# Performance work log

Measured on AMD Instinct MI355X. Metric: run time of the kernel, lower is better.

The kernel has to match this reference:

```python
import jax, jax.numpy as jnp
import numpy as np

EPS = 1e-5  # BatchNorm eps
B, T, D, H, C = 64, 1024, 128, 1024, 128


def _glorot(k, shape):
    lim = float(np.sqrt(6.0 / (shape[0] + shape[1])))
    return jax.random.uniform(k, shape, minval=-lim, maxval=lim, dtype=jnp.float32)


def _bn(x, g, b, m, v):
    # eval-mode BatchNorm1d over the channel (last) dim
    return (x - m) * (g * jax.lax.rsqrt(v + EPS)) + b


def _cell(x, h, c, Wih, Whh, bias):
    # PyTorch LSTM gate order: i, f, g, o
    z = x @ Wih.T + h @ Whh.T + bias
    i, f, g, o = jnp.split(z, 4, axis=-1)
    c = jax.nn.sigmoid(f) * c + jax.nn.sigmoid(i) * jnp.tanh(g)
    h = jax.nn.sigmoid(o) * jnp.tanh(c)
    return h, c


def setup_inputs() -> dict:
    key = jax.random.key(0)
    ks = jax.random.split(key, 24)
    d = {}
    d['x'] = jax.random.normal(ks[0], (B, T, D), dtype=jnp.float32)
    # input BN (eval mode running stats + affine)
    d['ibn_g'] = jnp.ones((D,), jnp.float32); d['ibn_b'] = jnp.zeros((D,), jnp.float32)
    d['ibn_m'] = 0.1 * jax.random.normal(ks[1], (D,), jnp.float32)
    d['ibn_v'] = jnp.ones((D,), jnp.float32)
    # encoder LSTM (2 layers)
    d['enc_Wih0'] = _glorot(ks[2], (4 * H, D)); d['enc_Whh0'] = _glorot(ks[3], (4 * H, H))
    d['enc_b0'] = jnp.zeros((4 * H,), jnp.float32)
    d['enc_Wih1'] = _glorot(ks[4], (4 * H, H)); d['enc_Whh1'] = _glorot(ks[5], (4 * H, H))
    d['enc_b1'] = jnp.zeros((4 * H,), jnp.float32)
    # decoder LSTM (2 layers), layer0 input = num_classes
    d['dec_Wih0'] = _glorot(ks[6], (4 * H, C)); d['dec_Whh0'] = _glorot(ks[7], (4 * H, H))
    d['dec_b0'] = jnp.zeros((4 * H,), jnp.float32)
    d['dec_Wih1'] = _glorot(ks[8], (4 * H, H)); d['dec_Whh1'] = _glorot(ks[9], (4 * H, H))
    d['dec_b1'] = jnp.zeros((4 * H,), jnp.float32)
    # hidden BN
    d['hbn_g'] = jnp.ones((H,), jnp.float32); d['hbn_b'] = jnp.zeros((H,), jnp.float32)
    d['hbn_m'] = 0.1 * jax.random.normal(ks[10], (H,), jnp.float32)
    d['hbn_v'] = jnp.ones((H,), jnp.float32)
    # fc head: Linear(H,H) -> BN -> ReLU -> (Dropout=identity in eval) -> Linear(H,C)
    d['fc1_W'] = _glorot(ks[11], (H, H)); d['fc1_b'] = jnp.zeros((H,), jnp.float32)
    d['fbn_g'] = jnp.ones((H,), jnp.float32); d['fbn_b'] = jnp.zeros((H,), jnp.float32)
    d['fbn_m'] = 0.1 * jax.random.normal(ks[12], (H,), jnp.float32)
    d['fbn_v'] = jnp.ones((H,), jnp.float32)
    d['fc2_W'] = _glorot(ks[13], (C, H)); d['fc2_b'] = jnp.zeros((C,), jnp.float32)
    return d


def reference(x, ibn_g, ibn_b, ibn_m, ibn_v,
              enc_Wih0, enc_Whh0, enc_b0, enc_Wih1, enc_Whh1, enc_b1,
              dec_Wih0, dec_Whh0, dec_b0, dec_Wih1, dec_Whh1, dec_b1,
              hbn_g, hbn_b, hbn_m, hbn_v,
              fc1_W, fc1_b, fbn_g, fbn_b, fbn_m, fbn_v, fc2_W, fc2_b):
    b, t, _ = x.shape
    h = enc_Whh0.shape[1]
    c_dim = fc2_W.shape[0]
    xn = _bn(x, ibn_g, ibn_b, ibn_m, ibn_v)  # (B,T,D), per-channel BN

    def enc_step(carry, xt):
        h0, c0, h1, c1 = carry
        h0, c0 = _cell(xt, h0, c0, enc_Wih0, enc_Whh0, enc_b0)
        h1, c1 = _cell(h0, h1, c1, enc_Wih1, enc_Whh1, enc_b1)
        return (h0, c0, h1, c1), None

    z = jnp.zeros((b, h), x.dtype)
    (h0, c0, h1, c1), _ = jax.lax.scan(enc_step, (z, z, z, z), jnp.swapaxes(xn, 0, 1))

    def dec_step(carry, _):
        d0, e0, d1, e1, y = carry
        d0, e0 = _cell(y, d0, e0, dec_Wih0, dec_Whh0, dec_b0)
        d1, e1 = _cell(d0, d1, e1, dec_Wih1, dec_Whh1, dec_b1)
        hb = _bn(d1, hbn_g, hbn_b, hbn_m, hbn_v)
        f1 = jax.nn.relu(_bn(hb @ fc1_W.T + fc1_b, fbn_g, fbn_b, fbn_m, fbn_v))
        pred = f1 @ fc2_W.T + fc2_b  # (B, C)
        return (d0, e0, d1, e1, pred), pred

    y0 = jnp.zeros((b, c_dim), x.dtype)
    _, preds = jax.lax.scan(dec_step, (h0, c0, h1, c1, y0), None, length=t)
    return jnp.swapaxes(preds, 0, 1)  # (B, T, C)
```

## Files before the change

### kernel.cpp

```cpp
#include <hip/hip_runtime.h>
#include <hip/hip_bf16.h>


typedef __hip_bfloat16 hbf16;
typedef __bf16 bf16x8 __attribute__((ext_vector_type(8)));
typedef float f32x4 __attribute__((ext_vector_type(4)));
#define DEVI static __device__ __forceinline__

#define PITCH 2056
#define PITCH0 1160
#define SLE 66048L
#define SLDATA 65536L

DEVI float sigf(float x) { return 1.0f / (1.0f + __expf(-x)); }

DEVI bf16x8 as_bf(f32x4 v) { union { f32x4 f; bf16x8 b; } u; u.f = v; return u.b; }

DEVI void st_u32_coh(void* p, unsigned int v) {
  __hip_atomic_store((unsigned int*)p, v, __ATOMIC_RELAXED, __HIP_MEMORY_SCOPE_AGENT);
}
DEVI void st_u64_coh(void* p, unsigned long long v) {
  __hip_atomic_store((unsigned long long*)p, v, __ATOMIC_RELAXED, __HIP_MEMORY_SCOPE_AGENT);
}
DEVI void st_f32_coh(float* p, float v) {
  __hip_atomic_store(p, v, __ATOMIC_RELAXED, __HIP_MEMORY_SCOPE_AGENT);
}
DEVI unsigned short bf_bits(float v) {
  union { __hip_bfloat16 b; unsigned short s; } u;
  u.b = __float2bfloat16(v);
  return u.s;
}

DEVI void ld32_wait(f32x4* b, const hbf16* ap) {
  asm volatile(
    "global_load_dwordx4 %0, %32, off sc0 sc1\n\t"
    "global_load_dwordx4 %1, %32, off offset:64 sc0 sc1\n\t"
    "global_load_dwordx4 %2, %32, off offset:128 sc0 sc1\n\t"
    "global_load_dwordx4 %3, %32, off offset:192 sc0 sc1\n\t"
    "global_load_dwordx4 %4, %32, off offset:256 sc0 sc1\n\t"
    "global_load_dwordx4 %5, %32, off offset:320 sc0 sc1\n\t"
    "global_load_dwordx4 %6, %32, off offset:384 sc0 sc1\n\t"
    "global_load_dwordx4 %7, %32, off offset:448 sc0 sc1\n\t"
    "global_load_dwordx4 %8, %32, off offset:512 sc0 sc1\n\t"
    "global_load_dwordx4 %9, %32, off offset:576 sc0 sc1\n\t"
    "global_load_dwordx4 %10, %32, off offset:640 sc0 sc1\n\t"
    "global_load_dwordx4 %11, %32, off offset:704 sc0 sc1\n\t"
    "global_load_dwordx4 %12, %32, off offset:768 sc0 sc1\n\t"
    "global_load_dwordx4 %13, %32, off offset:832 sc0 sc1\n\t"
    "global_load_dwordx4 %14, %32, off offset:896 sc0 sc1\n\t"
    "global_load_dwordx4 %15, %32, off offset:960 sc0 sc1\n\t"
    "global_load_dwordx4 %16, %32, off offset:1024 sc0 sc1\n\t"
    "global_load_dwordx4 %17, %32, off offset:1088 sc0 sc1\n\t"
    "global_load_dwordx4 %18, %32, off offset:1152 sc0 sc1\n\t"
    "global_load_dwordx4 %19, %32, off offset:1216 sc0 sc1\n\t"
    "global_load_dwordx4 %20, %32, off offset:1280 sc0 sc1\n\t"
    "global_load_dwordx4 %21, %32, off offset:1344 sc0 sc1\n\t"
    "global_load_dwordx4 %22, %32, off offset:1408 sc0 sc1\n\t"
    "global_load_dwordx4 %23, %32, off offset:1472 sc0 sc1\n\t"
    "global_load_dwordx4 %24, %32, off offset:1536 sc0 sc1\n\t"
    "global_load_dwordx4 %25, %32, off offset:1600 sc0 sc1\n\t"
    "global_load_dwordx4 %26, %32, off offset:1664 sc0 sc1\n\t"
    "global_load_dwordx4 %27, %32, off offset:1728 sc0 sc1\n\t"
    "global_load_dwordx4 %28, %32, off offset:1792 sc0 sc1\n\t"
    "global_load_dwordx4 %29, %32, off offset:1856 sc0 sc1\n\t"
    "global_load_dwordx4 %30, %32, off offset:1920 sc0 sc1\n\t"
    "global_load_dwordx4 %31, %32, off offset:1984 sc0 sc1\n\t"
    "s_waitcnt vmcnt(0)"
    : "=&v"(b[0]), "=&v"(b[1]), "=&v"(b[2]), "=&v"(b[3]),
      "=&v"(b[4]), "=&v"(b[5]), "=&v"(b[6]), "=&v"(b[7]),
      "=&v"(b[8]), "=&v"(b[9]), "=&v"(b[10]), "=&v"(b[11]),
      "=&v"(b[12]), "=&v"(b[13]), "=&v"(b[14]), "=&v"(b[15]),
      "=&v"(b[16]), "=&v"(b[17]), "=&v"(b[18]), "=&v"(b[19]),
      "=&v"(b[20]), "=&v"(b[21]), "=&v"(b[22]), "=&v"(b[23]),
      "=&v"(b[24]), "=&v"(b[25]), "=&v"(b[26]), "=&v"(b[27]),
      "=&v"(b[28]), "=&v"(b[29]), "=&v"(b[30]), "=&v"(b[31])
    : "v"(ap) : "memory");
}

DEVI void ld4x8_wait(f32x4* b, const hbf16* a0, const hbf16* a1,
                     const hbf16* a2, const hbf16* a3) {
  asm volatile(
    "global_load_dwordx4 %0, %32, off sc0 sc1\n\t"
    "global_load_dwordx4 %1, %32, off offset:64 sc0 sc1\n\t"
    "global_load_dwordx4 %2, %32, off offset:128 sc0 sc1\n\t"
    "global_load_dwordx4 %3, %32, off offset:192 sc0 sc1\n\t"
    "global_load_dwordx4 %4, %32, off offset:256 sc0 sc1\n\t"
    "global_load_dwordx4 %5, %32, off offset:320 sc0 sc1\n\t"
    "global_load_dwordx4 %6, %32, off offset:384 sc0 sc1\n\t"
    "global_load_dwordx4 %7, %32, off offset:448 sc0 sc1\n\t"
    "global_load_dwordx4 %8, %33, off sc0 sc1\n\t"
    "global_load_dwordx4 %9, %33, off offset:64 sc0 sc1\n\t"
    "global_load_dwordx4 %10, %33, off offset:128 sc0 sc1\n\t"
    "global_load_dwordx4 %11, %33, off offset:192 sc0 sc1\n\t"
    "global_load_dwordx4 %12, %33, off offset:256 sc0 sc1\n\t"
    "global_load_dwordx4 %13, %33, off offset:320 sc0 sc1\n\t"
    "global_load_dwordx4 %14, %33, off offset:384 sc0 sc1\n\t"
    "global_load_dwordx4 %15, %33, off offset:448 sc0 sc1\n\t"
    "global_load_dwordx4 %16, %34, off sc0 sc1\n\t"
    "global_load_dwordx4 %17, %34, off offset:64 sc0 sc1\n\t"
    "global_load_dwordx4 %18, %34, off offset:128 sc0 sc1\n\t"
    "global_load_dwordx4 %19, %34, off offset:192 sc0 sc1\n\t"
    "global_load_dwordx4 %20, %34, off offset:256 sc0 sc1\n\t"
    "global_load_dwordx4 %21, %34, off offset:320 sc0 sc1\n\t"
    "global_load_dwordx4 %22, %34, off offset:384 sc0 sc1\n\t"
    "global_load_dwordx4 %23, %34, off offset:448 sc0 sc1\n\t"
    "global_load_dwordx4 %24, %35, off sc0 sc1\n\t"
    "global_load_dwordx4 %25, %35, off offset:64 sc0 sc1\n\t"
    "global_load_dwordx4 %26, %35, off offset:128 sc0 sc1\n\t"
    "global_load_dwordx4 %27, %35, off offset:192 sc0 sc1\n\t"
    "global_load_dwordx4 %28, %35, off offset:256 sc0 sc1\n\t"
    "global_load_dwordx4 %29, %35, off offset:320 sc0 sc1\n\t"
    "global_load_dwordx4 %30, %35, off offset:384 sc0 sc1\n\t"
    "global_load_dwordx4 %31, %35, off offset:448 sc0 sc1\n\t"
    "s_waitcnt vmcnt(0)"
    : "=&v"(b[0]), "=&v"(b[1]), "=&v"(b[2]), "=&v"(b[3]),
      "=&v"(b[4]), "=&v"(b[5]), "=&v"(b[6]), "=&v"(b[7]),
      "=&v"(b[8]), "=&v"(b[9]), "=&v"(b[10]), "=&v"(b[11]),
      "=&v"(b[12]), "=&v"(b[13]), "=&v"(b[14]), "=&v"(b[15]),
      "=&v"(b[16]), "=&v"(b[17]), "=&v"(b[18]), "=&v"(b[19]),
      "=&v"(b[20]), "=&v"(b[21]), "=&v"(b[22]), "=&v"(b[23]),
      "=&v"(b[24]), "=&v"(b[25]), "=&v"(b[26]), "=&v"(b[27]),
      "=&v"(b[28]), "=&v"(b[29]), "=&v"(b[30]), "=&v"(b[31])
    : "v"(a0), "v"(a1), "v"(a2), "v"(a3) : "memory");
}

DEVI void gbar(int* cnt8, int e) {
  asm volatile("s_waitcnt vmcnt(0) lgkmcnt(0)" ::: "memory");
  __syncthreads();
  if (threadIdx.x == 0)
    __hip_atomic_fetch_add(&cnt8[(blockIdx.x & 7) * 16], 1,
                           __ATOMIC_RELAXED, __HIP_MEMORY_SCOPE_AGENT);
  if (threadIdx.x < 8) {
    while (__hip_atomic_load(&cnt8[threadIdx.x * 16], __ATOMIC_RELAXED,
                             __HIP_MEMORY_SCOPE_AGENT) < e * 32)
      __builtin_amdgcn_s_sleep(1);
  }
  __syncthreads();
}

DEVI void fill_w(hbf16* W, int pitch, int koff, const hbf16* __restrict__ Wg,
                 int Kg, int base_h) {
  for (int r = (int)(threadIdx.x >> 3); r < 32; r += 32) {
    int g = r >> 3, hc = r & 7;
    const hbf16* src = Wg + (long)(g * 1024 + base_h + hc) * Kg;
    hbf16* dst = W + r * pitch + koff;
    for (int k = (threadIdx.x & 7) * 8; k < Kg; k += 64)
      *reinterpret_cast<bf16x8*>(dst + k) =
          *reinterpret_cast<const bf16x8*>(src + k);
  }
}

DEVI void seg_asm(f32x4& a0, f32x4& a1, const hbf16* __restrict__ A, long lda,
                  const hbf16* W, int pitch, int koff, int w, int q, int r16) {
  const hbf16* ap = A + (long)(w * 16 + r16) * lda + q * 8;
  const hbf16* w0 = W + r16 * pitch + koff + q * 8;
  const hbf16* w1 = W + (16 + r16) * pitch + koff + q * 8;
  f32x4 b[32];
  ld32_wait(b, ap);
#pragma unroll
  for (int k = 0; k < 32; ++k) {
    bf16x8 av = as_bf(b[k]);
    bf16x8 b0 = *reinterpret_cast<const bf16x8*>(w0 + k * 32);
    bf16x8 b1 = *reinterpret_cast<const bf16x8*>(w1 + k * 32);
    a0 = __builtin_amdgcn_mfma_f32_16x16x32_bf16(av, b0, a0, 0, 0, 0);
    a1 = __builtin_amdgcn_mfma_f32_16x16x32_bf16(av, b1, a1, 0, 0, 0);
  }
}

DEVI void seg_pl(f32x4& a0, f32x4& a1, const hbf16* A,
                 const hbf16* W, int pitch, int koff, int w, int q, int r16) {
  const hbf16* ap = A + (long)(w * 16 + r16) * 1024L + q * 8;
  const hbf16* w0 = W + r16 * pitch + koff + q * 8;
  const hbf16* w1 = W + (16 + r16) * pitch + koff + q * 8;
#pragma unroll
  for (int k = 0; k < 32; ++k) {
    bf16x8 av = *reinterpret_cast<const bf16x8*>(ap + k * 32);
    bf16x8 b0 = *reinterpret_cast<const bf16x8*>(w0 + k * 32);
    bf16x8 b1 = *reinterpret_cast<const bf16x8*>(w1 + k * 32);
    a0 = __builtin_amdgcn_mfma_f32_16x16x32_bf16(av, b0, a0, 0, 0, 0);
    a1 = __builtin_amdgcn_mfma_f32_16x16x32_bf16(av, b1, a1, 0, 0, 0);
  }
}

DEVI void seg_x(f32x4& a0, f32x4& a1, const hbf16* __restrict__ A, long lda,
                const hbf16* W, int pitch, int w, int q, int r16) {
  const hbf16* ap = A + (long)(w * 16 + r16) * lda + q * 8;
  const hbf16* w0 = W + r16 * pitch + q * 8;
  const hbf16* w1 = W + (16 + r16) * pitch + q * 8;
#pragma unroll
  for (int k = 0; k < 128; k += 32) {
    bf16x8 av = *reinterpret_cast<const bf16x8*>(ap + k);
    bf16x8 b0 = *reinterpret_cast<const bf16x8*>(w0 + k);
    bf16x8 b1 = *reinterpret_cast<const bf16x8*>(w1 + k);
    a0 = __builtin_amdgcn_mfma_f32_16x16x32_bf16(av, b0, a0, 0, 0, 0);
    a1 = __builtin_amdgcn_mfma_f32_16x16x32_bf16(av, b1, a1, 0, 0, 0);
  }
}

DEVI void mm4_asm(f32x4* pa, const hbf16* __restrict__ abase, const bf16x8* fr) {
  f32x4 b[32];
  ld4x8_wait(b, abase, abase + 16384, abase + 32768, abase + 49152);
#pragma unroll
  for (int i = 0; i < 8; ++i)
#pragma unroll
    for (int mt = 0; mt < 4; ++mt)
      pa[mt] = __builtin_amdgcn_mfma_f32_16x16x32_bf16(
          as_bf(b[mt * 8 + i]), fr[i], pa[mt], 0, 0, 0);
}

DEVI void mm4_pl(f32x4* pa, const hbf16* abase, const bf16x8* fr) {
  f32x4 b[32];
#pragma unroll
  for (int mt = 0; mt < 4; ++mt)
#pragma unroll
    for (int i = 0; i < 8; ++i)
      b[mt * 8 + i] = *reinterpret_cast<const f32x4*>(
          reinterpret_cast<const char*>(abase + mt * 16384) + i * 64);
#pragma unroll
  for (int i = 0; i < 8; ++i)
#pragma unroll
    for (int mt = 0; mt < 4; ++mt)
      pa[mt] = __builtin_amdgcn_mfma_f32_16x16x32_bf16(
          as_bf(b[mt * 8 + i]), fr[i], pa[mt], 0, 0, 0);
}

DEVI void cell(f32x4 a0, f32x4 a1, float bb0, float bb1, float* cst,
               hbf16* hout, int base_h, int lane, int w) {
  int q = lane >> 4, c = lane & 15;
#pragma unroll
  for (int r = 0; r < 4; ++r) {
    float z0 = a0[r] + bb0;
    float z1 = a1[r] + bb1;
    float zf = __shfl(z0, lane | 8, 64);
    float zo = __shfl(z1, lane | 8, 64);
    float hv = 0.f;
    if (c < 8) {
      float cn = sigf(zf) * cst[r] + sigf(z0) * tanhf(z1);
      cst[r] = cn;
      hv = sigf(zo) * tanhf(cn);
    }
    unsigned short my = bf_bits(hv);
    unsigned short nb = (unsigned short)__shfl((int)my, lane ^ 1, 64);
    if (c < 8 && (c & 1) == 0) {
      unsigned int pk = (unsigned int)my | ((unsigned int)nb << 16);
      st_u32_coh(hout + (long)(w * 16 + q * 4 + r) * 1024 + base_h + c, pk);
    }
  }
}

DEVI void store_c(const float* cst, float* cbuf, int hcol_g, int lane, int w) {
  int q = lane >> 4, c = lane & 15;
  if (c < 8) {
#pragma unroll
    for (int r = 0; r < 4; ++r)
      st_f32_coh(&cbuf[(long)(w * 16 + q * 4 + r) * 1024 + hcol_g], cst[r]);
  }
}

template<int RING>
__global__ __launch_bounds__(256, 1) void k_enc(
    const hbf16* __restrict__ xb,
    const hbf16* __restrict__ Wih0f, const hbf16* __restrict__ Whh0,
    const hbf16* __restrict__ Wih1, const hbf16* __restrict__ Whh1,
    const float* __restrict__ b0f, const float* __restrict__ b1f,
    hbf16* h0_0, hbf16* h0_1, hbf16* h1_0, hbf16* h1_1,
    hbf16* rh0, hbf16* rh1,
    float* c0buf, float* c1buf, int* flags) {
  __shared__ hbf16 W[32 * PITCH];
  int wg = blockIdx.x, tid = threadIdx.x;
  int lane = tid & 63, w = tid >> 6, q = lane >> 4, c = lane & 15;
  bool isL0 = wg < 128;
  int cu = isL0 ? wg : wg - 128;
  int base_h = cu * 8;
  if (isL0) {
    fill_w(W, PITCH0, 0, Wih0f, 128, base_h);
    fill_w(W, PITCH0, 128, Whh0, 1024, base_h);
  } else {
    fill_w(W, PITCH, 0, Wih1, 1024, base_h);
    fill_w(W, PITCH, 1024, Whh1, 1024, base_h);
  }
  __syncthreads();
  const float* bias = isL0 ? b0f : b1f;
  float bb0 = bias[(c >> 3) * 1024 + base_h + (c & 7)];
  float bb1 = bias[(2 + (c >> 3)) * 1024 + base_h + (c & 7)];
  float cst[4] = {0.f, 0.f, 0.f, 0.f};
  int hcol_g = base_h + (c & 7);

  for (int t = 0; t <= 1024; ++t) {
    if (isL0) {
      if (t < 1024) {
        f32x4 a0 = {0.f,0.f,0.f,0.f}, a1 = {0.f,0.f,0.f,0.f};
        if constexpr (RING) {
          seg_pl(a0, a1, rh0 + (long)t * SLE, W, PITCH0, 128, w, q, c);
          seg_x(a0, a1, xb + (long)t * 128, 131072L, W, PITCH0, w, q, c);
          cell(a0, a1, bb0, bb1, cst, rh0 + (long)(t + 1) * SLE, base_h, lane, w);
        } else {
          const hbf16* h0r = (t & 1) ? h0_0 : h0_1;
          seg_asm(a0, a1, h0r, 1024L, W, PITCH0, 128, w, q, c);
          seg_x(a0, a1, xb + (long)t * 128, 131072L, W, PITCH0, w, q, c);
          hbf16* h0w = (t & 1) ? h0_1 : h0_0;
          cell(a0, a1, bb0, bb1, cst, h0w, base_h, lane, w);
        }
        if (t == 1023) store_c(cst, c0buf, hcol_g, lane, w);
      }
    } else {
      if (t >= 1) {
        f32x4 a0 = {0.f,0.f,0.f,0.f}, a1 = {0.f,0.f,0.f,0.f};
        if constexpr (RING) {
          seg_pl(a0, a1, rh0 + (long)t * SLE, W, PITCH, 0, w, q, c);
          seg_pl(a0, a1, rh1 + (long)(t - 1) * SLE, W, PITCH, 1024, w, q, c);
          cell(a0, a1, bb0, bb1, cst, rh1 + (long)t * SLE, base_h, lane, w);
        } else {
          const hbf16* h0r = (t & 1) ? h0_0 : h0_1;
          seg_asm(a0, a1, h0r, 1024L, W, PITCH, 0, w, q, c);
          const hbf16* h1r = (t & 1) ? h1_1 : h1_0;
          seg_asm(a0, a1, h1r, 1024L, W, PITCH, 1024, w, q, c);
          hbf16* h1w = (t & 1) ? h1_0 : h1_1;
          cell(a0, a1, bb0, bb1, cst, h1w, base_h, lane, w);
        }
        if (t == 1024) store_c(cst, c1buf, hcol_g, lane, w);
      }
    }
    if (t < 1024) gbar(flags, t + 1);
  }
}

template<int RING>
__global__ __launch_bounds__(256, 1) void k_dec(
    const hbf16* __restrict__ Wfold, const hbf16* __restrict__ Whh0d,
    const hbf16* __restrict__ Wih1d, const hbf16* __restrict__ Whh1d,
    const float* __restrict__ b0t, const float* __restrict__ b0p,
    const float* __restrict__ b1d,
    const hbf16* __restrict__ fc1Wf, const float* __restrict__ fc1bf,
    const float* __restrict__ fs2, const float* __restrict__ fadd2,
    const hbf16* __restrict__ fc2Wb, const float* __restrict__ fc2b,
    hbf16* d0_0, hbf16* d0_1, hbf16* d1_0, hbf16* d1_1, hbf16* f1b,
    hbf16* rf1, hbf16* rd0, hbf16* rd1,
    const hbf16* h0fin, const hbf16* h1fin,
    const float* __restrict__ c0buf, const float* __restrict__ c1buf,
    float* __restrict__ out, int* flags) {
  __shared__ hbf16 W[32 * PITCH];
  __shared__ float bounce[4][64][16];
  int wg = blockIdx.x, tid = threadIdx.x;
  int lane = tid & 63, w = tid >> 6, q = lane >> 4, c = lane & 15;
  bool isP1 = wg < 128;
  int cu = isP1 ? wg : wg - 128;
  int base_h = cu * 8;
  if (isP1) {
    fill_w(W, PITCH, 0, Wfold, 1024, base_h);
    fill_w(W, PITCH, 1024, Whh0d, 1024, base_h);
  } else {
    fill_w(W, PITCH, 0, Wih1d, 1024, base_h);
    fill_w(W, PITCH, 1024, Whh1d, 1024, base_h);
  }
  __syncthreads();
  int gi0 = (c >> 3) * 1024 + base_h + (c & 7);
  int gi1 = (2 + (c >> 3)) * 1024 + base_h + (c & 7);
  float bt0, bt1, bp0, bp1;
  if (isP1) { bt0 = b0t[gi0]; bt1 = b0t[gi1]; bp0 = b0p[gi0]; bp1 = b0p[gi1]; }
  else      { bt0 = b1d[gi0]; bt1 = b1d[gi1]; bp0 = bt0;      bp1 = bt1; }
  int hcol_g = base_h + (c & 7);
  float cst[4] = {0.f, 0.f, 0.f, 0.f};
  {
    const float* cb = isP1 ? c0buf : c1buf;
    if (c < 8) {
#pragma unroll
      for (int r = 0; r < 4; ++r)
        cst[r] = cb[(long)(w * 16 + q * 4 + r) * 1024 + hcol_g];
    }
  }
  bool isP3 = (wg < 64);
  bool isPred = (wg >= 128 && wg < 136);
  bf16x8 fr[8];
#pragma unroll
  for (int i = 0; i < 8; ++i) fr[i] = bf16x8{0,0,0,0,0,0,0,0};
  float e_b[4] = {0,0,0,0}, e_s[4] = {0,0,0,0}, e_a[4] = {0,0,0,0};
  int red_row = tid >> 2, red_c4 = (tid & 3) * 4;
  if (isP3) {
    const hbf16* fp = fc1Wf + (long)(wg * 16 + c) * 1024 + w * 256 + q * 8;
#pragma unroll
    for (int i = 0; i < 8; ++i) fr[i] = *reinterpret_cast<const bf16x8*>(fp + i * 32);
#pragma unroll
    for (int i = 0; i < 4; ++i) {
      int col = wg * 16 + red_c4 + i;
      e_b[i] = fc1bf[col]; e_s[i] = fs2[col]; e_a[i] = fadd2[col];
    }
  } else if (isPred) {
    const hbf16* fp = fc2Wb + (long)((wg - 128) * 16 + c) * 1024 + w * 256 + q * 8;
#pragma unroll
    for (int i = 0; i < 8; ++i) fr[i] = *reinterpret_cast<const bf16x8*>(fp + i * 32);
#pragma unroll
    for (int i = 0; i < 4; ++i) e_b[i] = fc2b[(wg - 128) * 16 + red_c4 + i];
  }

  f32x4 r0 = {0.f,0.f,0.f,0.f}, r1 = {0.f,0.f,0.f,0.f};

  for (int t = 0; t <= 1024; ++t) {
    if (isP1 && t < 1024) {
      f32x4 a0 = r0, a1 = r1;
      if (t > 0) {
        if constexpr (RING)
          seg_pl(a0, a1, rf1 + (long)(t - 1) * SLE, W, PITCH, 0, w, q, c);
        else
          seg_asm(a0, a1, f1b, 1024L, W, PITCH, 0, w, q, c);
      } else {
        if constexpr (RING)
          seg_pl(a0, a1, h0fin, W, PITCH, 1024, w, q, c);
        else
          seg_asm(a0, a1, d0_1, 1024L, W, PITCH, 1024, w, q, c);
      }
      float B0 = (t > 0) ? bt0 : bp0, B1 = (t > 0) ? bt1 : bp1;
      hbf16* d0w = RING ? (rd0 + (long)t * SLE) : ((t & 1) ? d0_1 : d0_0);
      cell(a0, a1, B0, B1, cst, d0w, base_h, lane, w);
    }
    if (!isP1 && t == 0) {
      if constexpr (RING)
        seg_pl(r0, r1, h1fin, W, PITCH, 1024, w, q, c);
      else
        seg_asm(r0, r1, d1_1, 1024L, W, PITCH, 1024, w, q, c);
    }
    if (isPred && t >= 1) {
      f32x4 pa[4] = {{0.f,0.f,0.f,0.f},{0.f,0.f,0.f,0.f},{0.f,0.f,0.f,0.f},{0.f,0.f,0.f,0.f}};
      if constexpr (RING)
        mm4_pl(pa, rf1 + (long)(t - 1) * SLE + (long)c * 1024 + w * 256 + q * 8, fr);
      else
        mm4_asm(pa, f1b + (long)c * 1024 + w * 256 + q * 8, fr);
#pragma unroll
      for (int mt = 0; mt < 4; ++mt)
#pragma unroll
        for (int r = 0; r < 4; ++r) bounce[w][mt * 16 + q * 4 + r][c] = pa[mt][r];
      __syncthreads();
#pragma unroll
      for (int i = 0; i < 4; ++i) {
        int cc = red_c4 + i;
        float s = bounce[0][red_row][cc] + bounce[1][red_row][cc] +
                  bounce[2][red_row][cc] + bounce[3][red_row][cc] + e_b[i];
        out[(long)red_row * 131072 + (long)(t - 1) * 128 + (wg - 128) * 16 + cc] = s;
      }
    }
    if (t == 1024) break;
    gbar(flags, 3 * t + 1);
    if (!isP1) {
      f32x4 a0 = r0, a1 = r1;
      if constexpr (RING) {
        seg_pl(a0, a1, rd0 + (long)t * SLE, W, PITCH, 0, w, q, c);
        cell(a0, a1, bt0, bt1, cst, rd1 + (long)t * SLE, base_h, lane, w);
      } else {
        const hbf16* d0c = (t & 1) ? d0_1 : d0_0;
        seg_asm(a0, a1, d0c, 1024L, W, PITCH, 0, w, q, c);
        hbf16* d1w = (t & 1) ? d1_1 : d1_0;
        cell(a0, a1, bt0, bt1, cst, d1w, base_h, lane, w);
      }
    } else if (isP3 && t < 1023) {
      r0 = f32x4{0.f,0.f,0.f,0.f}; r1 = f32x4{0.f,0.f,0.f,0.f};
      if constexpr (RING)
        seg_pl(r0, r1, rd0 + (long)t * SLE, W, PITCH, 1024, w, q, c);
      else {
        const hbf16* d0n = (t & 1) ? d0_1 : d0_0;
        seg_asm(r0, r1, d0n, 1024L, W, PITCH, 1024, w, q, c);
      }
    }
    gbar(flags, 3 * t + 2);
    if (isP3) {
      f32x4 pa[4] = {{0.f,0.f,0.f,0.f},{0.f,0.f,0.f,0.f},{0.f,0.f,0.f,0.f},{0.f,0.f,0.f,0.f}};
      if constexpr (RING)
        mm4_pl(pa, rd1 + (long)t * SLE + (long)c * 1024 + w * 256 + q * 8, fr);
      else {
        const hbf16* d1c = (t & 1) ? d1_1 : d1_0;
        mm4_asm(pa, d1c + (long)c * 1024 + w * 256 + q * 8, fr);
      }
#pragma unroll
      for (int mt = 0; mt < 4; ++mt)
#pragma unroll
        for (int r = 0; r < 4; ++r) bounce[w][mt * 16 + q * 4 + r][c] = pa[mt][r];
      __syncthreads();
#pragma unroll
      for (int i = 0; i < 4; ++i) {
        int cc = red_c4 + i;
        float s = bounce[0][red_row][cc] + bounce[1][red_row][cc] +
                  bounce[2][red_row][cc] + bounce[3][red_row][cc];
        float v = fmaxf((s + e_b[i]) * e_s[i] + e_a[i], 0.f);
        bounce[0][red_row][cc] = v;
      }
      {
        union { unsigned short s4[4]; unsigned long long u; } pk;
#pragma unroll
        for (int i = 0; i < 4; ++i) pk.s4[i] = bf_bits(bounce[0][red_row][red_c4 + i]);
        hbf16* f1dst = RING ? (rf1 + (long)t * SLE) : f1b;
        st_u64_coh(f1dst + (long)red_row * 1024 + wg * 16 + red_c4, pk.u);
      }
    } else if (isP1 && t < 1023) {
      r0 = f32x4{0.f,0.f,0.f,0.f}; r1 = f32x4{0.f,0.f,0.f,0.f};
      if constexpr (RING)
        seg_pl(r0, r1, rd0 + (long)t * SLE, W, PITCH, 1024, w, q, c);
      else {
        const hbf16* d0n = (t & 1) ? d0_1 : d0_0;
        seg_asm(r0, r1, d0n, 1024L, W, PITCH, 1024, w, q, c);
      }
    }
    if (!isP1 && t < 1023) {
      r0 = f32x4{0.f,0.f,0.f,0.f}; r1 = f32x4{0.f,0.f,0.f,0.f};
      if constexpr (RING)
        seg_pl(r0, r1, rd1 + (long)t * SLE, W, PITCH, 1024, w, q, c);
      else {
        const hbf16* d1n = (t & 1) ? d1_1 : d1_0;
        seg_asm(r0, r1, d1n, 1024L, W, PITCH, 1024, w, q, c);
      }
    }
    gbar(flags, 3 * t + 3);
  }
}


__global__ void k_cast_bf16(const float* __restrict__ s, hbf16* __restrict__ d, long n) {
  long i = (long)blockIdx.x * blockDim.x + threadIdx.x;
  long stride = (long)gridDim.x * blockDim.x;
  for (; i < n; i += stride) d[i] = __float2bfloat16(s[i]);
}

__global__ void k_prep_b0tot(const float* __restrict__ dec_b0, const float* __restrict__ dWih0,
                             const float* __restrict__ fc2b, float* __restrict__ b0d_tot) {
  int n = blockIdx.x * 256 + threadIdx.x;
  float acc = 0.f;
  for (int cc = 0; cc < 128; ++cc) acc += dWih0[n * 128 + cc] * fc2b[cc];
  b0d_tot[n] = dec_b0[n] + acc;
}

__global__ void k_fold_ih0(const float* __restrict__ g, const float* __restrict__ bb,
                           const float* __restrict__ m, const float* __restrict__ v,
                           const float* __restrict__ Wm, const float* __restrict__ b0,
                           hbf16* __restrict__ Wf, float* __restrict__ biasf) {
  int n = blockIdx.x * 256 + threadIdx.x;
  float acc = 0.f;
  for (int k = 0; k < 128; ++k) {
    float s = g[k] * rsqrtf(v[k] + 1e-5f);
    float tt = bb[k] - m[k] * s;
    float wv = Wm[n * 128 + k];
    Wf[n * 128 + k] = __float2bfloat16(wv * s);
    acc += tt * wv;
  }
  biasf[n] = b0[n] + acc;
}

__global__ void k_fold_fc1(const float* __restrict__ hg, const float* __restrict__ hb,
                           const float* __restrict__ hm, const float* __restrict__ hv,
                           const float* __restrict__ Wm, const float* __restrict__ fb,
                           const float* __restrict__ fg, const float* __restrict__ fbb,
                           const float* __restrict__ fm, const float* __restrict__ fv,
                           hbf16* __restrict__ Wf, float* __restrict__ bfo,
                           float* __restrict__ fs2, float* __restrict__ fadd2) {
  int n = blockIdx.x * 256 + threadIdx.x;
  float acc = 0.f;
  for (int k = 0; k < 1024; ++k) {
    float s = hg[k] * rsqrtf(hv[k] + 1e-5f);
    float tt = hb[k] - hm[k] * s;
    float wv = Wm[(long)n * 1024 + k];
    Wf[(long)n * 1024 + k] = __float2bfloat16(wv * s);
    acc += tt * wv;
  }
  bfo[n] = fb[n] + acc;
  float s2 = fg[n] * rsqrtf(fv[n] + 1e-5f);
  fs2[n] = s2;
  fadd2[n] = fbb[n] - fm[n] * s2;
}

__global__ void k_fold_wf(const float* __restrict__ Wih0d, const float* __restrict__ fc2W,
                          hbf16* __restrict__ Wfold) {
  long gid = (long)blockIdx.x * 256 + threadIdx.x;
  int n = (int)(gid >> 10), jcol = (int)(gid & 1023);
  float acc = 0.f;
  for (int cc = 0; cc < 128; ++cc)
    acc += Wih0d[n * 128 + cc] * fc2W[cc * 1024 + jcol];
  Wfold[gid] = __float2bfloat16(acc);
}


extern "C" void kernel_launch(void* const* d_in, const int* in_sizes, int n_in,
                              void* d_out, int out_size, void* d_ws, size_t ws_size,
                              hipStream_t stream) {
  (void)in_sizes; (void)n_in; (void)out_size;
  const float* x     = (const float*)d_in[0];
  const float* ibn_g = (const float*)d_in[1];
  const float* ibn_b = (const float*)d_in[2];
  const float* ibn_m = (const float*)d_in[3];
  const float* ibn_v = (const float*)d_in[4];
  const float* eWih0 = (const float*)d_in[5];
  const float* eWhh0 = (const float*)d_in[6];
  const float* e_b0  = (const float*)d_in[7];
  const float* eWih1 = (const float*)d_in[8];
  const float* eWhh1 = (const float*)d_in[9];
  const float* e_b1  = (const float*)d_in[10];
  const float* dWih0 = (const float*)d_in[11];
  const float* dWhh0 = (const float*)d_in[12];
  const float* d_b0  = (const float*)d_in[13];
  const float* dWih1 = (const float*)d_in[14];
  const float* dWhh1 = (const float*)d_in[15];
  const float* d_b1  = (const float*)d_in[16];
  const float* hbn_g = (const float*)d_in[17];
  const float* hbn_b = (const float*)d_in[18];
  const float* hbn_m = (const float*)d_in[19];
  const float* hbn_v = (const float*)d_in[20];
  const float* fc1_W = (const float*)d_in[21];
  const float* fc1_b = (const float*)d_in[22];
  const float* fbn_g = (const float*)d_in[23];
  const float* fbn_b = (const float*)d_in[24];
  const float* fbn_m = (const float*)d_in[25];
  const float* fbn_v = (const float*)d_in[26];
  const float* fc2_W = (const float*)d_in[27];
  const float* fc2_b = (const float*)d_in[28];
  float* out = (float*)d_out;

  char* p = (char*)d_ws;
  auto alloc = [&](size_t bytes) -> void* {
    void* r = (void*)p;
    p += (bytes + 255) & ~(size_t)255;
    return r;
  };
  hbf16* xb     = (hbf16*)alloc(64L * 1024 * 128 * 2);
  hbf16* Wih0f  = (hbf16*)alloc(4096L * 128 * 2);
  hbf16* Whh0e  = (hbf16*)alloc(4096L * 1024 * 2);
  hbf16* Wih1e  = (hbf16*)alloc(4096L * 1024 * 2);
  hbf16* Whh1e  = (hbf16*)alloc(4096L * 1024 * 2);
  hbf16* Wfold  = (hbf16*)alloc(4096L * 1024 * 2);
  hbf16* Whh0d  = (hbf16*)alloc(4096L * 1024 * 2);
  hbf16* Wih1d  = (hbf16*)alloc(4096L * 1024 * 2);
  hbf16* Whh1d  = (hbf16*)alloc(4096L * 1024 * 2);
  hbf16* fc1Wf  = (hbf16*)alloc(1024L * 1024 * 2);
  hbf16* fc2Wb  = (hbf16*)alloc(128L * 1024 * 2);
  float* bias0f = (float*)alloc(4096 * 4);
  float* b0dtot = (float*)alloc(4096 * 4);
  float* fc1bf  = (float*)alloc(1024 * 4);
  float* fs2    = (float*)alloc(1024 * 4);
  float* fadd2  = (float*)alloc(1024 * 4);
  char* st = p;
  hbf16* h0_0 = (hbf16*)alloc(64L * 1024 * 2);
  hbf16* h0_1 = (hbf16*)alloc(64L * 1024 * 2);
  hbf16* h1_0 = (hbf16*)alloc(64L * 1024 * 2);
  hbf16* h1_1 = (hbf16*)alloc(64L * 1024 * 2);
  float* c0b  = (float*)alloc(64L * 1024 * 4);
  float* c1b  = (float*)alloc(64L * 1024 * 4);
  hbf16* f1b  = (hbf16*)alloc(64L * 1024 * 2);
  int*   flagsE = (int*)alloc(256 * 4);
  int*   flagsD = (int*)alloc(256 * 4);
  size_t stbytes = (size_t)(p - st);

  hbf16* rh0 = (hbf16*)alloc(1025L * SLE * 2);
  hbf16* rh1 = (hbf16*)alloc(1025L * SLE * 2);
  hbf16* rf1 = (hbf16*)alloc(1024L * SLE * 2);
  hbf16* rd0 = (hbf16*)alloc(1024L * SLE * 2);
  hbf16* rd1 = (hbf16*)alloc(1024L * SLE * 2);
  size_t need = (size_t)(p - (char*)d_ws);
  bool use_ring = (ws_size >= need);

  hipMemsetAsync(st, 0, stbytes, stream);
  if (use_ring) {
    hipMemsetAsync(rh0, 0, SLDATA * 2, stream);
    hipMemsetAsync(rh1, 0, SLDATA * 2, stream);
  }

  k_cast_bf16<<<4096, 256, 0, stream>>>(x, xb, 64L * 1024 * 128);
  k_cast_bf16<<<2048, 256, 0, stream>>>(eWhh0, Whh0e, 4096L * 1024);
  k_cast_bf16<<<2048, 256, 0, stream>>>(eWih1, Wih1e, 4096L * 1024);
  k_cast_bf16<<<2048, 256, 0, stream>>>(eWhh1, Whh1e, 4096L * 1024);
  k_cast_bf16<<<2048, 256, 0, stream>>>(dWhh0, Whh0d, 4096L * 1024);
  k_cast_bf16<<<2048, 256, 0, stream>>>(dWih1, Wih1d, 4096L * 1024);
  k_cast_bf16<<<2048, 256, 0, stream>>>(dWhh1, Whh1d, 4096L * 1024);
  k_cast_bf16<<<512, 256, 0, stream>>>(fc2_W, fc2Wb, 128L * 1024);
  k_prep_b0tot<<<16, 256, 0, stream>>>(d_b0, dWih0, fc2_b, b0dtot);
  k_fold_ih0<<<16, 256, 0, stream>>>(ibn_g, ibn_b, ibn_m, ibn_v, eWih0, e_b0, Wih0f, bias0f);
  k_fold_fc1<<<4, 256, 0, stream>>>(hbn_g, hbn_b, hbn_m, hbn_v, fc1_W, fc1_b,
                                    fbn_g, fbn_b, fbn_m, fbn_v, fc1Wf, fc1bf, fs2, fadd2);
  k_fold_wf<<<16384, 256, 0, stream>>>(dWih0, fc2_W, Wfold);

  if (use_ring) {
    k_enc<1><<<256, 256, 0, stream>>>(xb, Wih0f, Whh0e, Wih1e, Whh1e, bias0f, e_b1,
                                      h0_0, h0_1, h1_0, h1_1, rh0, rh1,
                                      c0b, c1b, flagsE);
    k_dec<1><<<256, 256, 0, stream>>>(Wfold, Whh0d, Wih1d, Whh1d, b0dtot, d_b0, d_b1,
                                      fc1Wf, fc1bf, fs2, fadd2, fc2Wb, fc2_b,
                                      h0_0, h0_1, h1_0, h1_1, f1b,
                                      rf1, rd0, rd1,
                                      rh0 + 1024L * SLE, rh1 + 1024L * SLE,
                                      c0b, c1b, out, flagsD);
  } else {
    k_enc<0><<<256, 256, 0, stream>>>(xb, Wih0f, Whh0e, Wih1e, Whh1e, bias0f, e_b1,
                                      h0_0, h0_1, h1_0, h1_1, rh0, rh1,
                                      c0b, c1b, flagsE);
    k_dec<0><<<256, 256, 0, stream>>>(Wfold, Whh0d, Wih1d, Whh1d, b0dtot, d_b0, d_b1,
                                      fc1Wf, fc1bf, fs2, fadd2, fc2Wb, fc2_b,
                                      h0_0, h0_1, h1_0, h1_1, f1b,
                                      rf1, rd0, rd1,
                                      h0_1, h1_1,
                                      c0b, c1b, out, flagsD);
  }
}
```

Baseline: 39.69 ms.

## Use partial ring buffers when workspace cannot hold all five rings

Replaces the all-or-nothing ring-buffer choice with a graded scheme: up to three full-length ring buffers are allocated as workspace allows. The decoder reuses the encoder's rings for its d0/d1 states after the encoder finishes, so the full ring path needs only three buffers instead of five. Each hidden-state stream chooses per-template between the time-indexed ring (seg_pl, no reuse hazard) and the ping-pong buffers (seg_asm). This lets configurations with limited workspace still take the ring path for some streams. The cost is more template variants, plus a dependency on the decoder overwriting encoder ring slots only after the final encoder states have been read.

```diff
diff --git a/kernel.cpp b/kernel.cpp
--- a/kernel.cpp
+++ b/kernel.cpp
@@ -257,7 +257,7 @@
   }
 }
 
-template<int RING>
+template<int NR>
 __global__ __launch_bounds__(256, 1) void k_enc(
     const hbf16* __restrict__ xb,
     const hbf16* __restrict__ Wih0f, const hbf16* __restrict__ Whh0,
@@ -266,6 +266,7 @@
     hbf16* h0_0, hbf16* h0_1, hbf16* h1_0, hbf16* h1_1,
     hbf16* rh0, hbf16* rh1,
     float* c0buf, float* c1buf, int* flags) {
+  constexpr bool RH0 = NR >= 1, RH1 = NR >= 2;
   __shared__ hbf16 W[32 * PITCH];
   int wg = blockIdx.x, tid = threadIdx.x;
   int lane = tid & 63, w = tid >> 6, q = lane >> 4, c = lane & 15;
@@ -290,34 +291,36 @@
     if (isL0) {
       if (t < 1024) {
         f32x4 a0 = {0.f,0.f,0.f,0.f}, a1 = {0.f,0.f,0.f,0.f};
-        if constexpr (RING) {
+        if constexpr (RH0)
           seg_pl(a0, a1, rh0 + (long)t * SLE, W, PITCH0, 128, w, q, c);
-          seg_x(a0, a1, xb + (long)t * 128, 131072L, W, PITCH0, w, q, c);
-          cell(a0, a1, bb0, bb1, cst, rh0 + (long)(t + 1) * SLE, base_h, lane, w);
-        } else {
+        else {
           const hbf16* h0r = (t & 1) ? h0_0 : h0_1;
           seg_asm(a0, a1, h0r, 1024L, W, PITCH0, 128, w, q, c);
-          seg_x(a0, a1, xb + (long)t * 128, 131072L, W, PITCH0, w, q, c);
-          hbf16* h0w = (t & 1) ? h0_1 : h0_0;
-          cell(a0, a1, bb0, bb1, cst, h0w, base_h, lane, w);
         }
+        seg_x(a0, a1, xb + (long)t * 128, 131072L, W, PITCH0, w, q, c);
+        hbf16* h0w = RH0 ? (rh0 + (long)(t + 1) * SLE)
+                         : ((t & 1) ? h0_1 : h0_0);
+        cell(a0, a1, bb0, bb1, cst, h0w, base_h, lane, w);
         if (t == 1023) store_c(cst, c0buf, hcol_g, lane, w);
       }
     } else {
       if (t >= 1) {
         f32x4 a0 = {0.f,0.f,0.f,0.f}, a1 = {0.f,0.f,0.f,0.f};
-        if constexpr (RING) {
+        if constexpr (RH0)
           seg_pl(a0, a1, rh0 + (long)t * SLE, W, PITCH, 0, w, q, c);
-          seg_pl(a0, a1, rh1 + (long)(t - 1) * SLE, W, PITCH, 1024, w, q, c);
-          cell(a0, a1, bb0, bb1, cst, rh1 + (long)t * SLE, base_h, lane, w);
-        } else {
+        else {
           const hbf16* h0r = (t & 1) ? h0_0 : h0_1;
           seg_asm(a0, a1, h0r, 1024L, W, PITCH, 0, w, q, c);
+        }
+        if constexpr (RH1)
+          seg_pl(a0, a1, rh1 + (long)(t - 1) * SLE, W, PITCH, 1024, w, q, c);
+        else {
           const hbf16* h1r = (t & 1) ? h1_1 : h1_0;
           seg_asm(a0, a1, h1r, 1024L, W, PITCH, 1024, w, q, c);
-          hbf16* h1w = (t & 1) ? h1_0 : h1_1;
-          cell(a0, a1, bb0, bb1, cst, h1w, base_h, lane, w);
         }
+        hbf16* h1w = RH1 ? (rh1 + (long)t * SLE)
+                         : ((t & 1) ? h1_0 : h1_1);
+        cell(a0, a1, bb0, bb1, cst, h1w, base_h, lane, w);
         if (t == 1024) store_c(cst, c1buf, hcol_g, lane, w);
       }
     }
@@ -325,7 +328,7 @@
   }
 }
 
-template<int RING>
+template<int NR>
 __global__ __launch_bounds__(256, 1) void k_dec(
     const hbf16* __restrict__ Wfold, const hbf16* __restrict__ Whh0d,
     const hbf16* __restrict__ Wih1d, const hbf16* __restrict__ Whh1d,
@@ -339,6 +342,7 @@
     const hbf16* h0fin, const hbf16* h1fin,
     const float* __restrict__ c0buf, const float* __restrict__ c1buf,
     float* __restrict__ out, int* flags) {
+  constexpr bool RD0 = NR >= 1, RD1 = NR >= 2, RF1 = NR >= 3;
   __shared__ hbf16 W[32 * PITCH];
   __shared__ float bounce[4][64][16];
   int wg = blockIdx.x, tid = threadIdx.x;
@@ -399,29 +403,23 @@
     if (isP1 && t < 1024) {
       f32x4 a0 = r0, a1 = r1;
       if (t > 0) {
-        if constexpr (RING)
+        if constexpr (RF1)
           seg_pl(a0, a1, rf1 + (long)(t - 1) * SLE, W, PITCH, 0, w, q, c);
         else
           seg_asm(a0, a1, f1b, 1024L, W, PITCH, 0, w, q, c);
       } else {
-        if constexpr (RING)
-          seg_pl(a0, a1, h0fin, W, PITCH, 1024, w, q, c);
-        else
-          seg_asm(a0, a1, d0_1, 1024L, W, PITCH, 1024, w, q, c);
+        seg_pl(a0, a1, h0fin, W, PITCH, 1024, w, q, c);
       }
       float B0 = (t > 0) ? bt0 : bp0, B1 = (t > 0) ? bt1 : bp1;
-      hbf16* d0w = RING ? (rd0 + (long)t * SLE) : ((t & 1) ? d0_1 : d0_0);
+      hbf16* d0w = RD0 ? (rd0 + (long)t * SLE) : ((t & 1) ? d0_1 : d0_0);
       cell(a0, a1, B0, B1, cst, d0w, base_h, lane, w);
     }
     if (!isP1 && t == 0) {
-      if constexpr (RING)
-        seg_pl(r0, r1, h1fin, W, PITCH, 1024, w, q, c);
-      else
-        seg_asm(r0, r1, d1_1, 1024L, W, PITCH, 1024, w, q, c);
+      seg_pl(r0, r1, h1fin, W, PITCH, 1024, w, q, c);
     }
     if (isPred && t >= 1) {
       f32x4 pa[4] = {{0.f,0.f,0.f,0.f},{0.f,0.f,0.f,0.f},{0.f,0.f,0.f,0.f},{0.f,0.f,0.f,0.f}};
-      if constexpr (RING)
+      if constexpr (RF1)
         mm4_pl(pa, rf1 + (long)(t - 1) * SLE + (long)c * 1024 + w * 256 + q * 8, fr);
       else
         mm4_asm(pa, f1b + (long)c * 1024 + w * 256 + q * 8, fr);
@@ -442,18 +440,17 @@
     gbar(flags, 3 * t + 1);
     if (!isP1) {
       f32x4 a0 = r0, a1 = r1;
-      if constexpr (RING) {
+      if constexpr (RD0)
         seg_pl(a0, a1, rd0 + (long)t * SLE, W, PITCH, 0, w, q, c);
-        cell(a0, a1, bt0, bt1, cst, rd1 + (long)t * SLE, base_h, lane, w);
-      } else {
+      else {
         const hbf16* d0c = (t & 1) ? d0_1 : d0_0;
         seg_asm(a0, a1, d0c, 1024L, W, PITCH, 0, w, q, c);
-        hbf16* d1w = (t & 1) ? d1_1 : d1_0;
-        cell(a0, a1, bt0, bt1, cst, d1w, base_h, lane, w);
-      }
+      }
+      hbf16* d1w = RD1 ? (rd1 + (long)t * SLE) : ((t & 1) ? d1_1 : d1_0);
+      cell(a0, a1, bt0, bt1, cst, d1w, base_h, lane, w);
     } else if (isP3 && t < 1023) {
       r0 = f32x4{0.f,0.f,0.f,0.f}; r1 = f32x4{0.f,0.f,0.f,0.f};
-      if constexpr (RING)
+      if constexpr (RD0)
         seg_pl(r0, r1, rd0 + (long)t * SLE, W, PITCH, 1024, w, q, c);
       else {
         const hbf16* d0n = (t & 1) ? d0_1 : d0_0;
@@ -463,7 +460,7 @@
     gbar(flags, 3 * t + 2);
     if (isP3) {
       f32x4 pa[4] = {{0.f,0.f,0.f,0.f},{0.f,0.f,0.f,0.f},{0.f,0.f,0.f,0.f},{0.f,0.f,0.f,0.f}};
-      if constexpr (RING)
+      if constexpr (RD1)
         mm4_pl(pa, rd1 + (long)t * SLE + (long)c * 1024 + w * 256 + q * 8, fr);
       else {
         const hbf16* d1c = (t & 1) ? d1_1 : d1_0;
@@ -486,12 +483,12 @@
         union { unsigned short s4[4]; unsigned long long u; } pk;
 #pragma unroll
         for (int i = 0; i < 4; ++i) pk.s4[i] = bf_bits(bounce[0][red_row][red_c4 + i]);
-        hbf16* f1dst = RING ? (rf1 + (long)t * SLE) : f1b;
+        hbf16* f1dst = RF1 ? (rf1 + (long)t * SLE) : f1b;
         st_u64_coh(f1dst + (long)red_row * 1024 + wg * 16 + red_c4, pk.u);
       }
     } else if (isP1 && t < 1023) {
       r0 = f32x4{0.f,0.f,0.f,0.f}; r1 = f32x4{0.f,0.f,0.f,0.f};
-      if constexpr (RING)
+      if constexpr (RD0)
         seg_pl(r0, r1, rd0 + (long)t * SLE, W, PITCH, 1024, w, q, c);
       else {
         const hbf16* d0n = (t & 1) ? d0_1 : d0_0;
@@ -500,7 +497,7 @@
     }
     if (!isP1 && t < 1023) {
       r0 = f32x4{0.f,0.f,0.f,0.f}; r1 = f32x4{0.f,0.f,0.f,0.f};
-      if constexpr (RING)
+      if constexpr (RD1)
         seg_pl(r0, r1, rd1 + (long)t * SLE, W, PITCH, 1024, w, q, c);
       else {
         const hbf16* d1n = (t & 1) ? d1_1 : d1_0;
@@ -644,19 +641,19 @@
   int*   flagsD = (int*)alloc(256 * 4);
   size_t stbytes = (size_t)(p - st);
 
-  hbf16* rh0 = (hbf16*)alloc(1025L * SLE * 2);
-  hbf16* rh1 = (hbf16*)alloc(1025L * SLE * 2);
-  hbf16* rf1 = (hbf16*)alloc(1024L * SLE * 2);
-  hbf16* rd0 = (hbf16*)alloc(1024L * SLE * 2);
-  hbf16* rd1 = (hbf16*)alloc(1024L * SLE * 2);
-  size_t need = (size_t)(p - (char*)d_ws);
-  bool use_ring = (ws_size >= need);
+  const size_t ringBytes = 1025L * SLE * 2;
+  hbf16* ring[3] = {nullptr, nullptr, nullptr};
+  int NR = 0;
+  for (int i = 0; i < 3; ++i) {
+    if ((size_t)(p - (char*)d_ws) + ringBytes <= ws_size) {
+      ring[i] = (hbf16*)alloc(ringBytes);
+      NR = i + 1;
+    } else break;
+  }
 
   hipMemsetAsync(st, 0, stbytes, stream);
-  if (use_ring) {
-    hipMemsetAsync(rh0, 0, SLDATA * 2, stream);
-    hipMemsetAsync(rh1, 0, SLDATA * 2, stream);
-  }
+  if (NR >= 1) hipMemsetAsync(ring[0], 0, SLDATA * 2, stream);
+  if (NR >= 2) hipMemsetAsync(ring[1], 0, SLDATA * 2, stream);
 
   k_cast_bf16<<<4096, 256, 0, stream>>>(x, xb, 64L * 1024 * 128);
   k_cast_bf16<<<2048, 256, 0, stream>>>(eWhh0, Whh0e, 4096L * 1024);
@@ -672,25 +669,45 @@
                                     fbn_g, fbn_b, fbn_m, fbn_v, fc1Wf, fc1bf, fs2, fadd2);
   k_fold_wf<<<16384, 256, 0, stream>>>(dWih0, fc2_W, Wfold);
 
-  if (use_ring) {
-    k_enc<1><<<256, 256, 0, stream>>>(xb, Wih0f, Whh0e, Wih1e, Whh1e, bias0f, e_b1,
-                                      h0_0, h0_1, h1_0, h1_1, rh0, rh1,
-                                      c0b, c1b, flagsE);
-    k_dec<1><<<256, 256, 0, stream>>>(Wfold, Whh0d, Wih1d, Whh1d, b0dtot, d_b0, d_b1,
-                                      fc1Wf, fc1bf, fs2, fadd2, fc2Wb, fc2_b,
-                                      h0_0, h0_1, h1_0, h1_1, f1b,
-                                      rf1, rd0, rd1,
-                                      rh0 + 1024L * SLE, rh1 + 1024L * SLE,
-                                      c0b, c1b, out, flagsD);
-  } else {
-    k_enc<0><<<256, 256, 0, stream>>>(xb, Wih0f, Whh0e, Wih1e, Whh1e, bias0f, e_b1,
-                                      h0_0, h0_1, h1_0, h1_1, rh0, rh1,
-                                      c0b, c1b, flagsE);
-    k_dec<0><<<256, 256, 0, stream>>>(Wfold, Whh0d, Wih1d, Whh1d, b0dtot, d_b0, d_b1,
-                                      fc1Wf, fc1bf, fs2, fadd2, fc2Wb, fc2_b,
-                                      h0_0, h0_1, h1_0, h1_1, f1b,
-                                      rf1, rd0, rd1,
-                                      h0_1, h1_1,
-                                      c0b, c1b, out, flagsD);
-  }
-}
+  hbf16* rh0 = ring[0] ? ring[0] : f1b;
+  hbf16* rh1 = ring[1] ? ring[1] : f1b;
+  hbf16* rd0 = rh0, *rd1 = rh1;
+  hbf16* rf1 = ring[2] ? ring[2] : f1b;
+  const hbf16* h0fin = (NR >= 1) ? ring[0] + 1024L * SLE : h0_1;
+  const hbf16* h1fin = (NR >= 2) ? ring[1] + 1024L * SLE : h1_1;
+
+  switch (NR) {
+    case 3:
+      k_enc<2><<<256, 256, 0, stream>>>(xb, Wih0f, Whh0e, Wih1e, Whh1e, bias0f, e_b1,
+                                        h0_0, h0_1, h1_0, h1_1, rh0, rh1, c0b, c1b, flagsE);
+      k_dec<3><<<256, 256, 0, stream>>>(Wfold, Whh0d, Wih1d, Whh1d, b0dtot, d_b0, d_b1,
+                                        fc1Wf, fc1bf, fs2, fadd2, fc2Wb, fc2_b,
+                                        h0_0, h0_1, h1_0, h1_1, f1b, rf1, rd0, rd1,
+                                        h0fin, h1fin, c0b, c1b, out, flagsD);
+      break;
+    case 2:
+      k_enc<2><<<256, 256, 0, stream>>>(xb, Wih0f, Whh0e, Wih1e, Whh1e, bias0f, e_b1,
+                                        h0_0, h0_1, h1_0, h1_1, rh0, rh1, c0b, c1b, flagsE);
+      k_dec<2><<<256, 256, 0, stream>>>(Wfold, Whh0d, Wih1d, Whh1d, b0dtot, d_b0, d_b1,
+                                        fc1Wf, fc1bf, fs2, fadd2, fc2Wb, fc2_b,
+                                        h0_0, h0_1, h1_0, h1_1, f1b, rf1, rd0, rd1,
+                                        h0fin, h1fin, c0b, c1b, out, flagsD);
+      break;
+    case 1:
+      k_enc<1><<<256, 256, 0, stream>>>(xb, Wih0f, Whh0e, Wih1e, Whh1e, bias0f, e_b1,
+                                        h0_0, h0_1, h1_0, h1_1, rh0, rh1, c0b, c1b, flagsE);
+      k_dec<1><<<256, 256, 0, stream>>>(Wfold, Whh0d, Wih1d, Whh1d, b0dtot, d_b0, d_b1,
+                                        fc1Wf, fc1bf, fs2, fadd2, fc2Wb, fc2_b,
+                                        h0_0, h0_1, h1_0, h1_1, f1b, rf1, rd0, rd1,
+                                        h0fin, h1fin, c0b, c1b, out, flagsD);
+      break;
+    default:
+      k_enc<0><<<256, 256, 0, stream>>>(xb, Wih0f, Whh0e, Wih1e, Whh1e, bias0f, e_b1,
+                                        h0_0, h0_1, h1_0, h1_1, rh0, rh1, c0b, c1b, flagsE);
+      k_dec<0><<<256, 256, 0, stream>>>(Wfold, Whh0d, Wih1d, Whh1d, b0dtot, d_b0, d_b1,
+                                        fc1Wf, fc1bf, fs2, fadd2, fc2Wb, fc2_b,
+                                        h0_0, h0_1, h1_0, h1_1, f1b, rf1, rd0, rd1,
+                                        h0fin, h1fin, c0b, c1b, out, flagsD);
+      break;
+  }
+}
```

Result: slower. 42.72 ms (+7.6%).
